# Kernel optimization log

Measured on AMD Instinct MI355X. Metric: run time of the kernel, lower is better.

Reference implementation:

```python
import jax, jax.numpy as jnp
import numpy as np

N_NODES = 50000
N_EDGES = 800000
IN_C = 256
HID_C = 256
OUT_C = 128
N_GRAPHS = 256


def setup_inputs() -> dict:
    key = jax.random.key(0)
    ks = jax.random.split(key, 12)
    x = jax.random.normal(ks[0], (N_NODES, IN_C), dtype=jnp.float32)
    src = jax.random.randint(ks[1], (N_EDGES,), 0, N_NODES, dtype=jnp.int32)
    dst = jnp.sort(jax.random.randint(ks[2], (N_EDGES,), 0, N_NODES, dtype=jnp.int32))
    p = jax.random.uniform(ks[3], (N_NODES,), dtype=jnp.float32)
    batch = jnp.sort(jax.random.randint(ks[4], (N_NODES,), 0, N_GRAPHS, dtype=jnp.int32))
    root_ptr = jax.random.randint(ks[5], (N_GRAPHS,), 0, N_NODES, dtype=jnp.int32)
    s1 = 1.0 / np.sqrt(IN_C)
    s2 = 1.0 / np.sqrt(HID_C)
    s3 = 1.0 / np.sqrt(2 * HID_C)
    Wl1 = jax.random.uniform(ks[6], (IN_C, HID_C), jnp.float32, -s1, s1)
    Wr1 = jax.random.uniform(ks[7], (IN_C, HID_C), jnp.float32, -s1, s1)
    b1 = jnp.zeros((HID_C,), jnp.float32)
    Wl2 = jax.random.uniform(ks[8], (HID_C, HID_C), jnp.float32, -s2, s2)
    Wr2 = jax.random.uniform(ks[9], (HID_C, HID_C), jnp.float32, -s2, s2)
    b2 = jnp.zeros((HID_C,), jnp.float32)
    Wlin = jax.random.uniform(ks[10], (2 * HID_C, OUT_C), jnp.float32, -s3, s3)
    blin = jax.random.uniform(ks[11], (OUT_C,), jnp.float32, -s3, s3)
    return {"x": x, "src": src, "dst": dst, "p": p, "batch": batch,
            "root_ptr": root_ptr, "num_graphs": N_GRAPHS,
            "Wl1": Wl1, "Wr1": Wr1, "b1": b1,
            "Wl2": Wl2, "Wr2": Wr2, "b2": b2,
            "Wlin": Wlin, "blin": blin}


def _sage_conv(x, src, dst, inv_deg, Wl, Wr, b):
    # mean aggregation of neighbor features: scatter-add then divide by degree
    agg = jax.ops.segment_sum(x[src], dst, num_segments=N_NODES)  # [N, d]
    agg = agg * inv_deg[:, None]
    return agg @ Wl + x @ Wr + b


def reference(x, src, dst, p, batch, root_ptr, num_graphs,
              Wl1, Wr1, b1, Wl2, Wr2, b2, Wlin, blin):
    # in-degree for mean aggregation (shared by both convs)
    deg = jax.ops.segment_sum(jnp.ones_like(dst, dtype=x.dtype), dst,
                              num_segments=N_NODES)
    inv_deg = jnp.where(deg > 0, 1.0 / jnp.maximum(deg, 1.0), 0.0)

    h = _sage_conv(x, src, dst, inv_deg, Wl1, Wr1, b1)
    h = jax.nn.relu(h)  # dropout is identity in eval mode
    h = _sage_conv(h, src, dst, inv_deg, Wl2, Wr2, b2)

    # masked mean pool of p-weighted features per graph
    pw = h * p[:, None]
    gsum = jax.ops.segment_sum(pw, batch, num_segments=num_graphs)
    gcnt = jax.ops.segment_sum(jnp.ones_like(p), batch, num_segments=num_graphs)
    gmean = gsum / jnp.maximum(gcnt, 1.0)[:, None]

    feat = jnp.concatenate([h[root_ptr], gmean], axis=-1)  # [G, 2*hid]
    return feat @ Wlin + blin
```

## Files before the change

### kernel.cpp

```cpp
#include <hip/hip_runtime.h>
#include <hip/hip_bf16.h>

#define N_NODES 50000
#define N_EDGES 800000
#define C_DIM   256
#define OUT_C   128
#define N_GRAPHS 256

typedef unsigned short ushort8 __attribute__((ext_vector_type(8)));
typedef __bf16         bf16x8  __attribute__((ext_vector_type(8)));
typedef float          f32x4   __attribute__((ext_vector_type(4)));

typedef __attribute__((address_space(1))) const unsigned int gu32;
typedef __attribute__((address_space(3))) unsigned int lu32;

#if __has_builtin(__builtin_amdgcn_sched_barrier)
#define SCHED_FENCE() __builtin_amdgcn_sched_barrier(0)
#else
#define SCHED_FENCE() ((void)0)
#endif

__device__ __forceinline__ float us2f(unsigned short u) {
    unsigned int x = ((unsigned int)u) << 16;
    return __builtin_bit_cast(float, x);
}
__device__ __forceinline__ unsigned short f2bf(float f) {
    unsigned int u = __builtin_bit_cast(unsigned int, f);
    u += 0x7fffu + ((u >> 16) & 1u);
    return (unsigned short)(u >> 16);
}

__device__ __forceinline__ int lower_bound_i(const int* __restrict__ a, int n, int v) {
    int lo = 0, hi = n;
    while (lo < hi) {
        int mid = (lo + hi) >> 1;
        if (a[mid] < v) lo = mid + 1; else hi = mid;
    }
    return lo;
}

__global__ void preprocess(const float* __restrict__ x, unsigned short* __restrict__ xb,
                           const float* __restrict__ W0, const float* __restrict__ W1,
                           const float* __restrict__ W2, const float* __restrict__ W3,
                           unsigned short* __restrict__ D0, unsigned short* __restrict__ D1,
                           unsigned short* __restrict__ D2, unsigned short* __restrict__ D3,
                           const int* __restrict__ dst, const int* __restrict__ batch,
                           int* __restrict__ row_ptr, int* __restrict__ graph_ptr,
                           float* __restrict__ inv_deg) {
    __shared__ float tile[64][65];
    int b = blockIdx.x;
    int t = threadIdx.x;
    if (b < 12500) {
        int i = b * 256 + t;
        float4 v = *(const float4*)(x + ((size_t)i << 2));
        ushort4 o;
        o.x = f2bf(v.x); o.y = f2bf(v.y); o.z = f2bf(v.z); o.w = f2bf(v.w);
        *(ushort4*)(xb + ((size_t)i << 2)) = o;
    } else if (b < 12564) {
        int b2 = b - 12500;
        const float* S; unsigned short* D;
        switch (b2 >> 4) {
            case 0: S = W0; D = D0; break;
            case 1: S = W1; D = D1; break;
            case 2: S = W2; D = D2; break;
            default: S = W3; D = D3; break;
        }
        int tl = b2 & 15;
        int kt = (tl >> 2) * 64, nt = (tl & 3) * 64;
#pragma unroll
        for (int j = 0; j < 16; ++j) {
            int idx = t + j * 256;
            int r = idx >> 6, c = idx & 63;
            tile[r][c] = S[(size_t)(kt + r) * 256 + nt + c];
        }
        __syncthreads();
#pragma unroll
        for (int j = 0; j < 16; ++j) {
            int idx = t + j * 256;
            int r = idx >> 6, c = idx & 63;
            D[(size_t)(nt + r) * 256 + kt + c] = f2bf(tile[c][r]);
        }
    } else {
        int i = (b - 12564) * 256 + t;
        if (i <= N_NODES) {
            int lb = lower_bound_i(dst, N_EDGES, i);
            row_ptr[i] = lb;
            if (i < N_NODES) {
                int ub = lower_bound_i(dst, N_EDGES, i + 1);
                int cnt = ub - lb;
                inv_deg[i] = (cnt > 0) ? (1.0f / (float)cnt) : 0.0f;
            }
        }
        if (i <= N_GRAPHS) graph_ptr[i] = lower_bound_i(batch, N_NODES, i);
    }
}

__global__ void aggregate(const unsigned short* __restrict__ X,
                          const int* __restrict__ src,
                          const int* __restrict__ row_ptr,
                          const float* __restrict__ inv_deg,
                          unsigned short* __restrict__ out) {
    int gw   = (blockIdx.x * blockDim.x + threadIdx.x) >> 6;
    int lane = threadIdx.x & 63;
    if (gw >= N_NODES) return;
    int e0 = row_ptr[gw], e1 = row_ptr[gw + 1];
    const int lo = lane << 2;
    float a0 = 0.f, a1 = 0.f, a2 = 0.f, a3 = 0.f;
    int e = e0;

    for (; e + 16 <= e1; e += 16) {
        ushort4 v[16];
#pragma unroll
        for (int j = 0; j < 16; ++j) {
            int s = __builtin_amdgcn_readfirstlane(src[e + j]);
            v[j] = *(const ushort4*)(X + ((size_t)s << 8) + lo);
        }
        SCHED_FENCE();
#pragma unroll
        for (int j = 0; j < 16; ++j) {
            a0 += us2f(v[j].x); a1 += us2f(v[j].y);
            a2 += us2f(v[j].z); a3 += us2f(v[j].w);
        }
    }
    int rem = e1 - e;
    if (rem > 0) {
        int cl = e1 - 1;
        ushort4 v[16]; float w[16];
#pragma unroll
        for (int j = 0; j < 16; ++j) {
            int ej = e + j;
            int ec = ej < cl ? ej : cl;
            w[j] = (ej < e1) ? 1.0f : 0.0f;
            int s = __builtin_amdgcn_readfirstlane(src[ec]);
            v[j] = *(const ushort4*)(X + ((size_t)s << 8) + lo);
        }
        SCHED_FENCE();
#pragma unroll
        for (int j = 0; j < 16; ++j) {
            a0 = fmaf(us2f(v[j].x), w[j], a0);
            a1 = fmaf(us2f(v[j].y), w[j], a1);
            a2 = fmaf(us2f(v[j].z), w[j], a2);
            a3 = fmaf(us2f(v[j].w), w[j], a3);
        }
    }

    float sc = inv_deg[gw];
    ushort4 o;
    o.x = f2bf(a0 * sc); o.y = f2bf(a1 * sc); o.z = f2bf(a2 * sc); o.w = f2bf(a3 * sc);
    *(ushort4*)(out + ((size_t)gw << 8) + lo) = o;
}

__global__ __launch_bounds__(512, 2)
void gemm_fused(const unsigned short* __restrict__ A1,
                const unsigned short* __restrict__ A2,
                const unsigned short* __restrict__ B1t,
                const unsigned short* __restrict__ B2t,
                const float* __restrict__ bias,
                unsigned short* __restrict__ C,
                int M, int do_relu) {
    __shared__ __align__(16) unsigned short As[8192];
    __shared__ __align__(16) unsigned short Bs[16384];

    const int t    = threadIdx.x;
    const int m0   = blockIdx.x * 128;
    const int lane = t & 63, wid = t >> 6;
    const int wm   = (wid >> 2) * 64;
    const int wn   = (wid & 3) * 64;
    const int lrow = lane & 15;
    const int kq   = lane >> 4;

    const f32x4 zero4 = {0.f, 0.f, 0.f, 0.f};
    f32x4 acc[4][4];
#pragma unroll
    for (int i = 0; i < 4; ++i)
#pragma unroll
        for (int j = 0; j < 4; ++j) acc[i][j] = zero4;

    for (int it = 0; it < 8; ++it) {
        const unsigned short* __restrict__ Ab = (it < 4) ? A1 : A2;
        const unsigned short* __restrict__ Bb = (it < 4) ? B1t : B2t;
        int ko = (it * 64) & 255;

#pragma unroll
        for (int i = 0; i < 2; ++i) {
            int q   = t + i * 512;
            int row = q >> 3;
            int kb  = (q & 7) ^ (row & 7);
            const unsigned short* ga = Ab + (size_t)(m0 + row) * 256 + ko + kb * 8;
            __builtin_amdgcn_global_load_lds((gu32*)ga, (lu32*)(As + q * 8), 16, 0, 0);
        }
#pragma unroll
        for (int i = 0; i < 4; ++i) {
            int q   = t + i * 512;
            int row = q >> 3;
            int kb  = (q & 7) ^ (row & 7);
            const unsigned short* gb = Bb + (size_t)row * 256 + ko + kb * 8;
            __builtin_amdgcn_global_load_lds((gu32*)gb, (lu32*)(Bs + q * 8), 16, 0, 0);
        }
        __syncthreads();

#pragma unroll
        for (int s = 0; s < 2; ++s) {
            int kqp = s * 4 + kq;
            bf16x8 af[4], bfr[4];
#pragma unroll
            for (int mi = 0; mi < 4; ++mi) {
                int r = wm + mi * 16 + lrow;
                int slot = r * 8 + (kqp ^ (lrow & 7));
                uint4 u = *(const uint4*)(As + slot * 8);
                af[mi] = __builtin_bit_cast(bf16x8, u);
            }
#pragma unroll
            for (int ni = 0; ni < 4; ++ni) {
                int r = wn + ni * 16 + lrow;
                int slot = r * 8 + (kqp ^ (lrow & 7));
                uint4 u = *(const uint4*)(Bs + slot * 8);
                bfr[ni] = __builtin_bit_cast(bf16x8, u);
            }
#pragma unroll
            for (int mi = 0; mi < 4; ++mi)
#pragma unroll
                for (int ni = 0; ni < 4; ++ni)
                    acc[mi][ni] = __builtin_amdgcn_mfma_f32_16x16x32_bf16(
                        af[mi], bfr[ni], acc[mi][ni], 0, 0, 0);
        }
        __syncthreads();
    }

    const int rbase = (lane >> 4) * 4;
#pragma unroll
    for (int ni = 0; ni < 4; ++ni) {
        int n  = wn + ni * 16 + lrow;
        float bv = bias[n];
#pragma unroll
        for (int mi = 0; mi < 4; ++mi) {
            int mb = m0 + wm + mi * 16 + rbase;
#pragma unroll
            for (int r = 0; r < 4; ++r) {
                int m = mb + r;
                if (m < M) {
                    float v = acc[mi][ni][r] + bv;
                    if (do_relu) v = fmaxf(v, 0.f);
                    C[(size_t)m * 256 + n] = f2bf(v);
                }
            }
        }
    }
}

__global__ void pool_final(const unsigned short* __restrict__ h2,
                           const float* __restrict__ p,
                           const int* __restrict__ graph_ptr,
                           const int* __restrict__ root_ptr,
                           const float* __restrict__ Wlin,
                           const float* __restrict__ blin,
                           float* __restrict__ out) {
    __shared__ float part[2][256];
    __shared__ float fl[512];
    int g = blockIdx.x;
    int t = threadIdx.x;
    int c = t & 255;
    int half = t >> 8;
    int s = graph_ptr[g], e = graph_ptr[g + 1];
    int mid = s + ((e - s) >> 1);
    int lo0 = half ? mid : s;
    int hi0 = half ? e : mid;

    float acc = 0.f;
    for (int n = lo0; n < hi0; n += 8) {
        int cl = hi0 - 1;
        float w[8]; unsigned short v[8];
#pragma unroll
        for (int j = 0; j < 8; ++j) {
            int nj = n + j;
            int ncj = nj < cl ? nj : cl;
            int nu = __builtin_amdgcn_readfirstlane(ncj);
            w[j] = (nj < hi0) ? p[nu] : 0.0f;
            v[j] = h2[(size_t)nu * 256 + c];
        }
        SCHED_FENCE();
#pragma unroll
        for (int j = 0; j < 8; ++j)
            acc = fmaf(us2f(v[j]), w[j], acc);
    }
    part[half][c] = acc;
    __syncthreads();

    if (half == 0) {
        float cnt = (float)(e - s);
        int root = root_ptr[g];
        fl[c]       = us2f(h2[(size_t)root * 256 + c]);
        fl[256 + c] = (part[0][c] + part[1][c]) / fmaxf(cnt, 1.0f);
    }
    __syncthreads();

    if (t < 128) {
        int o = t;
        float s0 = 0.f, s1 = 0.f, s2 = 0.f, s3 = 0.f;
        for (int k = 0; k < 512; k += 4) {
            s0 = fmaf(fl[k + 0], Wlin[(k + 0) * 128 + o], s0);
            s1 = fmaf(fl[k + 1], Wlin[(k + 1) * 128 + o], s1);
            s2 = fmaf(fl[k + 2], Wlin[(k + 2) * 128 + o], s2);
            s3 = fmaf(fl[k + 3], Wlin[(k + 3) * 128 + o], s3);
        }
        out[(size_t)g * 128 + o] = blin[o] + ((s0 + s1) + (s2 + s3));
    }
}

extern "C" void kernel_launch(void* const* d_in, const int* in_sizes, int n_in,
                              void* d_out, int out_size, void* d_ws, size_t ws_size,
                              hipStream_t stream) {
    const float* x        = (const float*)d_in[0];
    const int*   src      = (const int*)d_in[1];
    const int*   dst      = (const int*)d_in[2];
    const float* p        = (const float*)d_in[3];
    const int*   batch    = (const int*)d_in[4];
    const int*   root_ptr = (const int*)d_in[5];
    const float* Wl1  = (const float*)d_in[7];
    const float* Wr1  = (const float*)d_in[8];
    const float* b1   = (const float*)d_in[9];
    const float* Wl2  = (const float*)d_in[10];
    const float* Wr2  = (const float*)d_in[11];
    const float* b2   = (const float*)d_in[12];
    const float* Wlin = (const float*)d_in[13];
    const float* blin = (const float*)d_in[14];
    float* out = (float*)d_out;

    size_t off = 0;
    char* base = (char*)d_ws;
    auto alloc = [&](size_t bytes) -> void* {
        void* q = base + off;
        off += (bytes + 255) & ~(size_t)255;
        return q;
    };
    int*            row_ptr   = (int*)  alloc((N_NODES + 1) * sizeof(int));
    int*            graph_ptr = (int*)  alloc((N_GRAPHS + 1) * sizeof(int));
    float*          inv_deg   = (float*)alloc(N_NODES * sizeof(float));
    unsigned short* Wl1t = (unsigned short*)alloc(256 * 256 * 2);
    unsigned short* Wr1t = (unsigned short*)alloc(256 * 256 * 2);
    unsigned short* Wl2t = (unsigned short*)alloc(256 * 256 * 2);
    unsigned short* Wr2t = (unsigned short*)alloc(256 * 256 * 2);
    unsigned short* xb   = (unsigned short*)alloc((size_t)N_NODES * 256 * 2);
    unsigned short* aggb = (unsigned short*)alloc((size_t)N_NODES * 256 * 2);
    unsigned short* h1   = (unsigned short*)alloc((size_t)N_NODES * 256 * 2);
    unsigned short* h2   = (unsigned short*)alloc((size_t)N_NODES * 256 * 2);
    (void)ws_size; (void)n_in; (void)in_sizes; (void)out_size;

    preprocess<<<12760, 256, 0, stream>>>(x, xb, Wl1, Wr1, Wl2, Wr2,
                                          Wl1t, Wr1t, Wl2t, Wr2t,
                                          dst, batch, row_ptr, graph_ptr, inv_deg);

    dim3 ggrid((N_NODES + 127) / 128);

    aggregate<<<N_NODES / 4, 256, 0, stream>>>(xb, src, row_ptr, inv_deg, aggb);
    gemm_fused<<<ggrid, 512, 0, stream>>>(aggb, xb, Wl1t, Wr1t, b1, h1, N_NODES, 1);

    aggregate<<<N_NODES / 4, 256, 0, stream>>>(h1, src, row_ptr, inv_deg, aggb);
    gemm_fused<<<ggrid, 512, 0, stream>>>(aggb, h1, Wl2t, Wr2t, b2, h2, N_NODES, 0);

    pool_final<<<N_GRAPHS, 512, 0, stream>>>(h2, p, graph_ptr, root_ptr,
                                             Wlin, blin, out);
}
```

Before: 314.4 us.

## Fuse neighbor aggregation and SAGE GEMM into one kernel per layer

Merges the gather-mean aggregation and the dual-weight GEMM into a single kernel. Each 32-row block aggregates its nodes into LDS and then runs MFMA directly against both weight matrices. This removes the round trip of the intermediate aggregate buffer through global memory and drops two launches. In exchange, the weights and self features are read straight from global memory without LDS staging, so every block re-reads the full weight matrices, and the smaller M tile lowers reuse per weight load.

```diff
diff --git a/kernel.cpp b/kernel.cpp
--- a/kernel.cpp
+++ b/kernel.cpp
@@ -7,12 +7,8 @@
 #define OUT_C   128
 #define N_GRAPHS 256
 
-typedef unsigned short ushort8 __attribute__((ext_vector_type(8)));
 typedef __bf16         bf16x8  __attribute__((ext_vector_type(8)));
 typedef float          f32x4   __attribute__((ext_vector_type(4)));
-
-typedef __attribute__((address_space(1))) const unsigned int gu32;
-typedef __attribute__((address_space(3))) unsigned int lu32;
 
 #if __has_builtin(__builtin_amdgcn_sched_barrier)
 #define SCHED_FENCE() __builtin_amdgcn_sched_barrier(0)
@@ -95,153 +91,144 @@
     }
 }
 
-__global__ void aggregate(const unsigned short* __restrict__ X,
-                          const int* __restrict__ src,
-                          const int* __restrict__ row_ptr,
-                          const float* __restrict__ inv_deg,
-                          unsigned short* __restrict__ out) {
-    int gw   = (blockIdx.x * blockDim.x + threadIdx.x) >> 6;
-    int lane = threadIdx.x & 63;
-    if (gw >= N_NODES) return;
-    int e0 = row_ptr[gw], e1 = row_ptr[gw + 1];
-    const int lo = lane << 2;
-    float a0 = 0.f, a1 = 0.f, a2 = 0.f, a3 = 0.f;
-    int e = e0;
-
-    for (; e + 16 <= e1; e += 16) {
-        ushort4 v[16];
-#pragma unroll
-        for (int j = 0; j < 16; ++j) {
-            int s = __builtin_amdgcn_readfirstlane(src[e + j]);
-            v[j] = *(const ushort4*)(X + ((size_t)s << 8) + lo);
-        }
-        SCHED_FENCE();
-#pragma unroll
-        for (int j = 0; j < 16; ++j) {
-            a0 += us2f(v[j].x); a1 += us2f(v[j].y);
-            a2 += us2f(v[j].z); a3 += us2f(v[j].w);
-        }
-    }
-    int rem = e1 - e;
-    if (rem > 0) {
-        int cl = e1 - 1;
-        ushort4 v[16]; float w[16];
-#pragma unroll
-        for (int j = 0; j < 16; ++j) {
-            int ej = e + j;
-            int ec = ej < cl ? ej : cl;
-            w[j] = (ej < e1) ? 1.0f : 0.0f;
-            int s = __builtin_amdgcn_readfirstlane(src[ec]);
-            v[j] = *(const ushort4*)(X + ((size_t)s << 8) + lo);
-        }
-        SCHED_FENCE();
-#pragma unroll
-        for (int j = 0; j < 16; ++j) {
-            a0 = fmaf(us2f(v[j].x), w[j], a0);
-            a1 = fmaf(us2f(v[j].y), w[j], a1);
-            a2 = fmaf(us2f(v[j].z), w[j], a2);
-            a3 = fmaf(us2f(v[j].w), w[j], a3);
-        }
-    }
-
-    float sc = inv_deg[gw];
-    ushort4 o;
-    o.x = f2bf(a0 * sc); o.y = f2bf(a1 * sc); o.z = f2bf(a2 * sc); o.w = f2bf(a3 * sc);
-    *(ushort4*)(out + ((size_t)gw << 8) + lo) = o;
-}
-
-__global__ __launch_bounds__(512, 2)
-void gemm_fused(const unsigned short* __restrict__ A1,
-                const unsigned short* __restrict__ A2,
+__global__ __launch_bounds__(256, 4)
+void sage_fused(const unsigned short* __restrict__ X,
+                const int* __restrict__ src,
+                const int* __restrict__ row_ptr,
+                const float* __restrict__ inv_deg,
                 const unsigned short* __restrict__ B1t,
                 const unsigned short* __restrict__ B2t,
                 const float* __restrict__ bias,
                 unsigned short* __restrict__ C,
-                int M, int do_relu) {
-    __shared__ __align__(16) unsigned short As[8192];
-    __shared__ __align__(16) unsigned short Bs[16384];
+                int do_relu) {
+    __shared__ __align__(16) unsigned short Agg[32 * 256];
 
     const int t    = threadIdx.x;
-    const int m0   = blockIdx.x * 128;
-    const int lane = t & 63, wid = t >> 6;
-    const int wm   = (wid >> 2) * 64;
-    const int wn   = (wid & 3) * 64;
+    const int lane = t & 63;
+    const int wid  = t >> 6;
+    const int m0   = blockIdx.x * 32;
+
+    {
+        const int lo = lane << 2;
+#pragma unroll 1
+        for (int i = 0; i < 8; ++i) {
+            const int lr   = (wid << 3) + i;
+            const int node = m0 + lr;
+            float a0 = 0.f, a1 = 0.f, a2 = 0.f, a3 = 0.f, sc = 0.f;
+            if (node < N_NODES) {
+                const int e0 = row_ptr[node], e1 = row_ptr[node + 1];
+                int e = e0;
+                for (; e + 16 <= e1; e += 16) {
+                    ushort4 v[16];
+#pragma unroll
+                    for (int j = 0; j < 16; ++j) {
+                        int s = __builtin_amdgcn_readfirstlane(src[e + j]);
+                        v[j] = *(const ushort4*)(X + ((size_t)s << 8) + lo);
+                    }
+                    SCHED_FENCE();
+#pragma unroll
+                    for (int j = 0; j < 16; ++j) {
+                        a0 += us2f(v[j].x); a1 += us2f(v[j].y);
+                        a2 += us2f(v[j].z); a3 += us2f(v[j].w);
+                    }
+                }
+                int rem = e1 - e;
+                if (rem > 0) {
+                    int cl = e1 - 1;
+                    ushort4 v[16]; float w[16];
+#pragma unroll
+                    for (int j = 0; j < 16; ++j) {
+                        int ej = e + j;
+                        int ec = ej < cl ? ej : cl;
+                        w[j] = (ej < e1) ? 1.0f : 0.0f;
+                        int s = __builtin_amdgcn_readfirstlane(src[ec]);
+                        v[j] = *(const ushort4*)(X + ((size_t)s << 8) + lo);
+                    }
+                    SCHED_FENCE();
+#pragma unroll
+                    for (int j = 0; j < 16; ++j) {
+                        a0 = fmaf(us2f(v[j].x), w[j], a0);
+                        a1 = fmaf(us2f(v[j].y), w[j], a1);
+                        a2 = fmaf(us2f(v[j].z), w[j], a2);
+                        a3 = fmaf(us2f(v[j].w), w[j], a3);
+                    }
+                }
+                sc = inv_deg[node];
+            }
+            ushort4 o;
+            o.x = f2bf(a0 * sc); o.y = f2bf(a1 * sc);
+            o.z = f2bf(a2 * sc); o.w = f2bf(a3 * sc);
+            const int cw  = lane >> 1;
+            const int off = (lr << 8) + (((cw ^ (lr & 7)) << 3) | ((lane & 1) << 2));
+            *(ushort4*)(&Agg[off]) = o;
+        }
+    }
+    __syncthreads();
+
     const int lrow = lane & 15;
     const int kq   = lane >> 4;
+    const int wn   = wid << 6;
 
     const f32x4 zero4 = {0.f, 0.f, 0.f, 0.f};
-    f32x4 acc[4][4];
-#pragma unroll
-    for (int i = 0; i < 4; ++i)
-#pragma unroll
-        for (int j = 0; j < 4; ++j) acc[i][j] = zero4;
-
-    for (int it = 0; it < 8; ++it) {
-        const unsigned short* __restrict__ Ab = (it < 4) ? A1 : A2;
-        const unsigned short* __restrict__ Bb = (it < 4) ? B1t : B2t;
-        int ko = (it * 64) & 255;
-
-#pragma unroll
-        for (int i = 0; i < 2; ++i) {
-            int q   = t + i * 512;
-            int row = q >> 3;
-            int kb  = (q & 7) ^ (row & 7);
-            const unsigned short* ga = Ab + (size_t)(m0 + row) * 256 + ko + kb * 8;
-            __builtin_amdgcn_global_load_lds((gu32*)ga, (lu32*)(As + q * 8), 16, 0, 0);
-        }
-#pragma unroll
-        for (int i = 0; i < 4; ++i) {
-            int q   = t + i * 512;
-            int row = q >> 3;
-            int kb  = (q & 7) ^ (row & 7);
-            const unsigned short* gb = Bb + (size_t)row * 256 + ko + kb * 8;
-            __builtin_amdgcn_global_load_lds((gu32*)gb, (lu32*)(Bs + q * 8), 16, 0, 0);
-        }
-        __syncthreads();
-
+    f32x4 acc[2][4];
+#pragma unroll
+    for (int mi = 0; mi < 2; ++mi)
+#pragma unroll
+        for (int ni = 0; ni < 4; ++ni) acc[mi][ni] = zero4;
+
+#pragma unroll
+    for (int it = 0; it < 4; ++it) {
 #pragma unroll
         for (int s = 0; s < 2; ++s) {
-            int kqp = s * 4 + kq;
-            bf16x8 af[4], bfr[4];
-#pragma unroll
-            for (int mi = 0; mi < 4; ++mi) {
-                int r = wm + mi * 16 + lrow;
-                int slot = r * 8 + (kqp ^ (lrow & 7));
-                uint4 u = *(const uint4*)(As + slot * 8);
-                af[mi] = __builtin_bit_cast(bf16x8, u);
+            const int c    = it * 8 + s * 4 + kq;
+            const int koff = it * 64 + s * 32 + kq * 8;
+            bf16x8 af1[2], af2[2], b1f[4], b2f[4];
+#pragma unroll
+            for (int mi = 0; mi < 2; ++mi) {
+                const int r = mi * 16 + lrow;
+                uint4 u = *(const uint4*)(&Agg[(r << 8) + ((c ^ (r & 7)) << 3)]);
+                af1[mi] = __builtin_bit_cast(bf16x8, u);
+                int gr = m0 + r;
+                if (gr > N_NODES - 1) gr = N_NODES - 1;
+                uint4 u2 = *(const uint4*)(X + ((size_t)gr << 8) + koff);
+                af2[mi] = __builtin_bit_cast(bf16x8, u2);
             }
 #pragma unroll
             for (int ni = 0; ni < 4; ++ni) {
-                int r = wn + ni * 16 + lrow;
-                int slot = r * 8 + (kqp ^ (lrow & 7));
-                uint4 u = *(const uint4*)(Bs + slot * 8);
-                bfr[ni] = __builtin_bit_cast(bf16x8, u);
-            }
-#pragma unroll
-            for (int mi = 0; mi < 4; ++mi)
-#pragma unroll
-                for (int ni = 0; ni < 4; ++ni)
+                const int n = wn + ni * 16 + lrow;
+                b1f[ni] = __builtin_bit_cast(bf16x8,
+                            *(const uint4*)(B1t + ((size_t)n << 8) + koff));
+                b2f[ni] = __builtin_bit_cast(bf16x8,
+                            *(const uint4*)(B2t + ((size_t)n << 8) + koff));
+            }
+#pragma unroll
+            for (int mi = 0; mi < 2; ++mi)
+#pragma unroll
+                for (int ni = 0; ni < 4; ++ni) {
                     acc[mi][ni] = __builtin_amdgcn_mfma_f32_16x16x32_bf16(
-                        af[mi], bfr[ni], acc[mi][ni], 0, 0, 0);
-        }
-        __syncthreads();
-    }
-
-    const int rbase = (lane >> 4) * 4;
+                        af1[mi], b1f[ni], acc[mi][ni], 0, 0, 0);
+                    acc[mi][ni] = __builtin_amdgcn_mfma_f32_16x16x32_bf16(
+                        af2[mi], b2f[ni], acc[mi][ni], 0, 0, 0);
+                }
+            SCHED_FENCE();
+        }
+    }
+
+    const int rbase = (lane >> 4) << 2;
 #pragma unroll
     for (int ni = 0; ni < 4; ++ni) {
-        int n  = wn + ni * 16 + lrow;
-        float bv = bias[n];
-#pragma unroll
-        for (int mi = 0; mi < 4; ++mi) {
-            int mb = m0 + wm + mi * 16 + rbase;
+        const int n  = wn + ni * 16 + lrow;
+        const float bv = bias[n];
+#pragma unroll
+        for (int mi = 0; mi < 2; ++mi) {
+            const int mb = m0 + mi * 16 + rbase;
 #pragma unroll
             for (int r = 0; r < 4; ++r) {
-                int m = mb + r;
-                if (m < M) {
+                const int m = mb + r;
+                if (m < N_NODES) {
                     float v = acc[mi][ni][r] + bv;
                     if (do_relu) v = fmaxf(v, 0.f);
-                    C[(size_t)m * 256 + n] = f2bf(v);
+                    C[((size_t)m << 8) + n] = f2bf(v);
                 }
             }
         }
@@ -341,7 +328,6 @@
     unsigned short* Wl2t = (unsigned short*)alloc(256 * 256 * 2);
     unsigned short* Wr2t = (unsigned short*)alloc(256 * 256 * 2);
     unsigned short* xb   = (unsigned short*)alloc((size_t)N_NODES * 256 * 2);
-    unsigned short* aggb = (unsigned short*)alloc((size_t)N_NODES * 256 * 2);
     unsigned short* h1   = (unsigned short*)alloc((size_t)N_NODES * 256 * 2);
     unsigned short* h2   = (unsigned short*)alloc((size_t)N_NODES * 256 * 2);
     (void)ws_size; (void)n_in; (void)in_sizes; (void)out_size;
@@ -350,13 +336,12 @@
                                           Wl1t, Wr1t, Wl2t, Wr2t,
                                           dst, batch, row_ptr, graph_ptr, inv_deg);
 
-    dim3 ggrid((N_NODES + 127) / 128);
-
-    aggregate<<<N_NODES / 4, 256, 0, stream>>>(xb, src, row_ptr, inv_deg, aggb);
-    gemm_fused<<<ggrid, 512, 0, stream>>>(aggb, xb, Wl1t, Wr1t, b1, h1, N_NODES, 1);
-
-    aggregate<<<N_NODES / 4, 256, 0, stream>>>(h1, src, row_ptr, inv_deg, aggb);
-    gemm_fused<<<ggrid, 512, 0, stream>>>(aggb, h1, Wl2t, Wr2t, b2, h2, N_NODES, 0);
+    dim3 fgrid((N_NODES + 31) / 32);
+
+    sage_fused<<<fgrid, 256, 0, stream>>>(xb, src, row_ptr, inv_deg,
+                                          Wl1t, Wr1t, b1, h1, 1);
+    sage_fused<<<fgrid, 256, 0, stream>>>(h1, src, row_ptr, inv_deg,
+                                          Wl2t, Wr2t, b2, h2, 0);
 
     pool_final<<<N_GRAPHS, 512, 0, stream>>>(h2, p, graph_ptr, root_ptr,
                                              Wlin, blin, out);
```

Measured after the change: 411.8 us. 1.31x slower.

## Replace LDS-staged GEMM with direct global-to-register MFMA tiles

Applied to the files above, without the earlier changes.

Rewrites the fused dual GEMM so each wave loads A and B fragments straight from global memory into registers, with no LDS staging and no barriers. Blocks shrink to 64 rows and 256 threads, each wave covering 64 output columns. This removes the LDS round trip and the syncthreads stalls, but the four waves now each re-read the same A rows and there is no cross-wave reuse through shared memory. Out-of-range rows are clamped to the last row instead of padded.

```diff
diff --git a/kernel.cpp b/kernel.cpp
--- a/kernel.cpp
+++ b/kernel.cpp
@@ -7,12 +7,8 @@
 #define OUT_C   128
 #define N_GRAPHS 256
 
-typedef unsigned short ushort8 __attribute__((ext_vector_type(8)));
 typedef __bf16         bf16x8  __attribute__((ext_vector_type(8)));
 typedef float          f32x4   __attribute__((ext_vector_type(4)));
-
-typedef __attribute__((address_space(1))) const unsigned int gu32;
-typedef __attribute__((address_space(3))) unsigned int lu32;
 
 #if __has_builtin(__builtin_amdgcn_sched_barrier)
 #define SCHED_FENCE() __builtin_amdgcn_sched_barrier(0)
@@ -150,98 +146,79 @@
     *(ushort4*)(out + ((size_t)gw << 8) + lo) = o;
 }
 
-__global__ __launch_bounds__(512, 2)
-void gemm_fused(const unsigned short* __restrict__ A1,
-                const unsigned short* __restrict__ A2,
-                const unsigned short* __restrict__ B1t,
-                const unsigned short* __restrict__ B2t,
-                const float* __restrict__ bias,
-                unsigned short* __restrict__ C,
-                int M, int do_relu) {
-    __shared__ __align__(16) unsigned short As[8192];
-    __shared__ __align__(16) unsigned short Bs[16384];
-
+__global__ __launch_bounds__(256, 4)
+void gemm_dual(const unsigned short* __restrict__ A1,
+               const unsigned short* __restrict__ A2,
+               const unsigned short* __restrict__ B1t,
+               const unsigned short* __restrict__ B2t,
+               const float* __restrict__ bias,
+               unsigned short* __restrict__ C,
+               int M, int do_relu) {
     const int t    = threadIdx.x;
-    const int m0   = blockIdx.x * 128;
-    const int lane = t & 63, wid = t >> 6;
-    const int wm   = (wid >> 2) * 64;
-    const int wn   = (wid & 3) * 64;
+    const int lane = t & 63;
+    const int wid  = t >> 6;
+    const int m0   = blockIdx.x * 64;
     const int lrow = lane & 15;
     const int kq   = lane >> 4;
+    const int wn   = wid << 6;
 
     const f32x4 zero4 = {0.f, 0.f, 0.f, 0.f};
     f32x4 acc[4][4];
 #pragma unroll
-    for (int i = 0; i < 4; ++i)
-#pragma unroll
-        for (int j = 0; j < 4; ++j) acc[i][j] = zero4;
-
-    for (int it = 0; it < 8; ++it) {
-        const unsigned short* __restrict__ Ab = (it < 4) ? A1 : A2;
-        const unsigned short* __restrict__ Bb = (it < 4) ? B1t : B2t;
-        int ko = (it * 64) & 255;
-
-#pragma unroll
-        for (int i = 0; i < 2; ++i) {
-            int q   = t + i * 512;
-            int row = q >> 3;
-            int kb  = (q & 7) ^ (row & 7);
-            const unsigned short* ga = Ab + (size_t)(m0 + row) * 256 + ko + kb * 8;
-            __builtin_amdgcn_global_load_lds((gu32*)ga, (lu32*)(As + q * 8), 16, 0, 0);
-        }
-#pragma unroll
-        for (int i = 0; i < 4; ++i) {
-            int q   = t + i * 512;
-            int row = q >> 3;
-            int kb  = (q & 7) ^ (row & 7);
-            const unsigned short* gb = Bb + (size_t)row * 256 + ko + kb * 8;
-            __builtin_amdgcn_global_load_lds((gu32*)gb, (lu32*)(Bs + q * 8), 16, 0, 0);
-        }
-        __syncthreads();
-
-#pragma unroll
-        for (int s = 0; s < 2; ++s) {
-            int kqp = s * 4 + kq;
-            bf16x8 af[4], bfr[4];
-#pragma unroll
-            for (int mi = 0; mi < 4; ++mi) {
-                int r = wm + mi * 16 + lrow;
-                int slot = r * 8 + (kqp ^ (lrow & 7));
-                uint4 u = *(const uint4*)(As + slot * 8);
-                af[mi] = __builtin_bit_cast(bf16x8, u);
-            }
+    for (int mi = 0; mi < 4; ++mi)
+#pragma unroll
+        for (int ni = 0; ni < 4; ++ni) acc[mi][ni] = zero4;
+
+    int rr[4];
+#pragma unroll
+    for (int mi = 0; mi < 4; ++mi) {
+        int r = m0 + mi * 16 + lrow;
+        rr[mi] = (r < M) ? r : (M - 1);
+    }
+
+#pragma unroll
+    for (int half = 0; half < 2; ++half) {
+        const unsigned short* __restrict__ A = half ? A2 : A1;
+        const unsigned short* __restrict__ B = half ? B2t : B1t;
+#pragma unroll
+        for (int ks = 0; ks < 8; ++ks) {
+            const int koff = ks * 32 + kq * 8;
+            bf16x8 af[4], bf[4];
+#pragma unroll
+            for (int mi = 0; mi < 4; ++mi)
+                af[mi] = __builtin_bit_cast(bf16x8,
+                           *(const uint4*)(A + ((size_t)rr[mi] << 8) + koff));
 #pragma unroll
             for (int ni = 0; ni < 4; ++ni) {
-                int r = wn + ni * 16 + lrow;
-                int slot = r * 8 + (kqp ^ (lrow & 7));
-                uint4 u = *(const uint4*)(Bs + slot * 8);
-                bfr[ni] = __builtin_bit_cast(bf16x8, u);
+                const int n = wn + ni * 16 + lrow;
+                bf[ni] = __builtin_bit_cast(bf16x8,
+                           *(const uint4*)(B + ((size_t)n << 8) + koff));
             }
 #pragma unroll
             for (int mi = 0; mi < 4; ++mi)
 #pragma unroll
                 for (int ni = 0; ni < 4; ++ni)
                     acc[mi][ni] = __builtin_amdgcn_mfma_f32_16x16x32_bf16(
-                        af[mi], bfr[ni], acc[mi][ni], 0, 0, 0);
-        }
-        __syncthreads();
-    }
-
-    const int rbase = (lane >> 4) * 4;
+                        af[mi], bf[ni], acc[mi][ni], 0, 0, 0);
+            SCHED_FENCE();
+        }
+    }
+
+    const int rbase = (lane >> 4) << 2;
 #pragma unroll
     for (int ni = 0; ni < 4; ++ni) {
-        int n  = wn + ni * 16 + lrow;
-        float bv = bias[n];
+        const int n  = wn + ni * 16 + lrow;
+        const float bv = bias[n];
 #pragma unroll
         for (int mi = 0; mi < 4; ++mi) {
-            int mb = m0 + wm + mi * 16 + rbase;
+            const int mb = m0 + mi * 16 + rbase;
 #pragma unroll
             for (int r = 0; r < 4; ++r) {
-                int m = mb + r;
+                const int m = mb + r;
                 if (m < M) {
                     float v = acc[mi][ni][r] + bv;
                     if (do_relu) v = fmaxf(v, 0.f);
-                    C[(size_t)m * 256 + n] = f2bf(v);
+                    C[((size_t)m << 8) + n] = f2bf(v);
                 }
             }
         }
@@ -350,13 +327,13 @@
                                           Wl1t, Wr1t, Wl2t, Wr2t,
                                           dst, batch, row_ptr, graph_ptr, inv_deg);
 
-    dim3 ggrid((N_NODES + 127) / 128);
+    dim3 ggrid((N_NODES + 63) / 64);
 
     aggregate<<<N_NODES / 4, 256, 0, stream>>>(xb, src, row_ptr, inv_deg, aggb);
-    gemm_fused<<<ggrid, 512, 0, stream>>>(aggb, xb, Wl1t, Wr1t, b1, h1, N_NODES, 1);
+    gemm_dual<<<ggrid, 256, 0, stream>>>(aggb, xb, Wl1t, Wr1t, b1, h1, N_NODES, 1);
 
     aggregate<<<N_NODES / 4, 256, 0, stream>>>(h1, src, row_ptr, inv_deg, aggb);
-    gemm_fused<<<ggrid, 512, 0, stream>>>(aggb, h1, Wl2t, Wr2t, b2, h2, N_NODES, 0);
+    gemm_dual<<<ggrid, 256, 0, stream>>>(aggb, h1, Wl2t, Wr2t, b2, h2, N_NODES, 0);
 
     pool_final<<<N_GRAPHS, 512, 0, stream>>>(h2, p, graph_ptr, root_ptr,
                                              Wlin, blin, out);
```

New measurement: 403.1 us. +28.2%, slower.

## Double-buffer GEMM LDS tiles and shrink block to 64 rows with 4 waves

Applied to the files above, without the earlier changes.

Restructures the fused SAGE GEMM so each block handles 64 rows with 256 threads (four waves split across N) and double-buffers the A and B tiles in LDS. The next K-slice is prefetched with global_load_lds while MFMAs run on the current one, using an explicit vmcnt wait and raw s_barrier instead of full __syncthreads. This is meant to hide global load latency behind compute. In exchange each block reloads the full B tile for only 64 rows, doubling weight traffic per output row, and LDS use grows to about 80 KB per block, which may limit occupancy. The M tail also reads past N_NODES rows in the last block, as before.

```diff
diff --git a/kernel.cpp b/kernel.cpp
--- a/kernel.cpp
+++ b/kernel.cpp
@@ -7,7 +7,6 @@
 #define OUT_C   128
 #define N_GRAPHS 256
 
-typedef unsigned short ushort8 __attribute__((ext_vector_type(8)));
 typedef __bf16         bf16x8  __attribute__((ext_vector_type(8)));
 typedef float          f32x4   __attribute__((ext_vector_type(4)));
 
@@ -150,7 +149,29 @@
     *(ushort4*)(out + ((size_t)gw << 8) + lo) = o;
 }
 
-__global__ __launch_bounds__(512, 2)
+__device__ __forceinline__ void stage_tile(unsigned short* As, unsigned short* Bs,
+                                           int t, int m0, int ko,
+                                           const unsigned short* __restrict__ Ab,
+                                           const unsigned short* __restrict__ Bb) {
+#pragma unroll
+    for (int i = 0; i < 2; ++i) {
+        int q   = t + i * 256;
+        int row = q >> 3;
+        int kb  = (q & 7) ^ (row & 7);
+        const unsigned short* ga = Ab + (size_t)(m0 + row) * 256 + ko + kb * 8;
+        __builtin_amdgcn_global_load_lds((gu32*)ga, (lu32*)(As + q * 8), 16, 0, 0);
+    }
+#pragma unroll
+    for (int i = 0; i < 8; ++i) {
+        int q   = t + i * 256;
+        int row = q >> 3;
+        int kb  = (q & 7) ^ (row & 7);
+        const unsigned short* gb = Bb + (size_t)row * 256 + ko + kb * 8;
+        __builtin_amdgcn_global_load_lds((gu32*)gb, (lu32*)(Bs + q * 8), 16, 0, 0);
+    }
+}
+
+__global__ __launch_bounds__(256, 2)
 void gemm_fused(const unsigned short* __restrict__ A1,
                 const unsigned short* __restrict__ A2,
                 const unsigned short* __restrict__ B1t,
@@ -158,14 +179,13 @@
                 const float* __restrict__ bias,
                 unsigned short* __restrict__ C,
                 int M, int do_relu) {
-    __shared__ __align__(16) unsigned short As[8192];
-    __shared__ __align__(16) unsigned short Bs[16384];
+    __shared__ __align__(16) unsigned short As[2][4096];
+    __shared__ __align__(16) unsigned short Bs[2][16384];
 
     const int t    = threadIdx.x;
-    const int m0   = blockIdx.x * 128;
     const int lane = t & 63, wid = t >> 6;
-    const int wm   = (wid >> 2) * 64;
-    const int wn   = (wid & 3) * 64;
+    const int wn   = wid << 6;
+    const int m0   = blockIdx.x * 64;
     const int lrow = lane & 15;
     const int kq   = lane >> 4;
 
@@ -176,28 +196,23 @@
 #pragma unroll
         for (int j = 0; j < 4; ++j) acc[i][j] = zero4;
 
+    stage_tile(As[0], Bs[0], t, m0, 0, A1, B1t);
+    SCHED_FENCE();
+
+#pragma unroll
     for (int it = 0; it < 8; ++it) {
-        const unsigned short* __restrict__ Ab = (it < 4) ? A1 : A2;
-        const unsigned short* __restrict__ Bb = (it < 4) ? B1t : B2t;
-        int ko = (it * 64) & 255;
-
-#pragma unroll
-        for (int i = 0; i < 2; ++i) {
-            int q   = t + i * 512;
-            int row = q >> 3;
-            int kb  = (q & 7) ^ (row & 7);
-            const unsigned short* ga = Ab + (size_t)(m0 + row) * 256 + ko + kb * 8;
-            __builtin_amdgcn_global_load_lds((gu32*)ga, (lu32*)(As + q * 8), 16, 0, 0);
-        }
-#pragma unroll
-        for (int i = 0; i < 4; ++i) {
-            int q   = t + i * 512;
-            int row = q >> 3;
-            int kb  = (q & 7) ^ (row & 7);
-            const unsigned short* gb = Bb + (size_t)row * 256 + ko + kb * 8;
-            __builtin_amdgcn_global_load_lds((gu32*)gb, (lu32*)(Bs + q * 8), 16, 0, 0);
-        }
-        __syncthreads();
+        const int cur = it & 1;
+        if (it < 7) {
+            const int nit = it + 1;
+            const unsigned short* Ab = (nit < 4) ? A1 : A2;
+            const unsigned short* Bb = (nit < 4) ? B1t : B2t;
+            stage_tile(As[cur ^ 1], Bs[cur ^ 1], t, m0, (nit * 64) & 255, Ab, Bb);
+            asm volatile("s_waitcnt vmcnt(10)" ::: "memory");
+        } else {
+            asm volatile("s_waitcnt vmcnt(0)" ::: "memory");
+        }
+        __builtin_amdgcn_s_barrier();
+        SCHED_FENCE();
 
 #pragma unroll
         for (int s = 0; s < 2; ++s) {
@@ -205,16 +220,16 @@
             bf16x8 af[4], bfr[4];
 #pragma unroll
             for (int mi = 0; mi < 4; ++mi) {
-                int r = wm + mi * 16 + lrow;
+                int r = mi * 16 + lrow;
                 int slot = r * 8 + (kqp ^ (lrow & 7));
-                uint4 u = *(const uint4*)(As + slot * 8);
+                uint4 u = *(const uint4*)(As[cur] + slot * 8);
                 af[mi] = __builtin_bit_cast(bf16x8, u);
             }
 #pragma unroll
             for (int ni = 0; ni < 4; ++ni) {
                 int r = wn + ni * 16 + lrow;
                 int slot = r * 8 + (kqp ^ (lrow & 7));
-                uint4 u = *(const uint4*)(Bs + slot * 8);
+                uint4 u = *(const uint4*)(Bs[cur] + slot * 8);
                 bfr[ni] = __builtin_bit_cast(bf16x8, u);
             }
 #pragma unroll
@@ -224,7 +239,8 @@
                     acc[mi][ni] = __builtin_amdgcn_mfma_f32_16x16x32_bf16(
                         af[mi], bfr[ni], acc[mi][ni], 0, 0, 0);
         }
-        __syncthreads();
+        SCHED_FENCE();
+        __builtin_amdgcn_s_barrier();
     }
 
     const int rbase = (lane >> 4) * 4;
@@ -234,7 +250,7 @@
         float bv = bias[n];
 #pragma unroll
         for (int mi = 0; mi < 4; ++mi) {
-            int mb = m0 + wm + mi * 16 + rbase;
+            int mb = m0 + mi * 16 + rbase;
 #pragma unroll
             for (int r = 0; r < 4; ++r) {
                 int m = mb + r;
@@ -350,13 +366,13 @@
                                           Wl1t, Wr1t, Wl2t, Wr2t,
                                           dst, batch, row_ptr, graph_ptr, inv_deg);
 
-    dim3 ggrid((N_NODES + 127) / 128);
+    dim3 ggrid((N_NODES + 63) / 64);
 
     aggregate<<<N_NODES / 4, 256, 0, stream>>>(xb, src, row_ptr, inv_deg, aggb);
-    gemm_fused<<<ggrid, 512, 0, stream>>>(aggb, xb, Wl1t, Wr1t, b1, h1, N_NODES, 1);
+    gemm_fused<<<ggrid, 256, 0, stream>>>(aggb, xb, Wl1t, Wr1t, b1, h1, N_NODES, 1);
 
     aggregate<<<N_NODES / 4, 256, 0, stream>>>(h1, src, row_ptr, inv_deg, aggb);
-    gemm_fused<<<ggrid, 512, 0, stream>>>(aggb, h1, Wl2t, Wr2t, b2, h2, N_NODES, 0);
+    gemm_fused<<<ggrid, 256, 0, stream>>>(aggb, h1, Wl2t, Wr2t, b2, h2, N_NODES, 0);
 
     pool_final<<<N_GRAPHS, 512, 0, stream>>>(h2, p, graph_ptr, root_ptr,
                                              Wlin, blin, out);
```

After: 348.0 us. 1.11x slower.
